# Optimization experiments

Measured on AMD Instinct MI355X. Metric: run time of the kernel, lower is better.

## Reference

```python
import jax, jax.numpy as jnp
import numpy as np

EMB_LEN = 16384
EMB_DIM = 128
BETA = 0.25
WEIGHT_DECAY = 0.01


def resize_linear(x, axis, out_size):
    # PyTorch (tri)linear interpolation, align_corners=False, separable per axis.
    in_size = x.shape[axis]
    if in_size == out_size:
        return x
    src = (jnp.arange(out_size, dtype=jnp.float32) + 0.5) * (in_size / out_size) - 0.5
    src = jnp.clip(src, 0.0, in_size - 1.0)
    i0 = jnp.floor(src).astype(jnp.int32)
    i1 = jnp.minimum(i0 + 1, in_size - 1)
    w1 = src - i0.astype(jnp.float32)
    x0 = jnp.take(x, i0, axis=axis)
    x1 = jnp.take(x, i1, axis=axis)
    bshape = [1] * x.ndim
    bshape[axis] = out_size
    w1 = w1.reshape(bshape)
    return x0 * (1.0 - w1) + x1 * w1


def setup_inputs() -> dict:
    key = jax.random.key(0)
    k1, k2 = jax.random.split(key)
    b, c, h, w = 16384, 16, 2, 4  # h*w must equal 8 (see shape analysis)
    z = jax.random.normal(k1, (b, c, h, w), dtype=jnp.float32)
    emb_weight = jax.random.uniform(
        k2, (EMB_LEN, EMB_DIM), dtype=jnp.float32,
        minval=-1.0 / EMB_LEN, maxval=1.0 / EMB_LEN)
    return {"z": z, "emb_weight": emb_weight}


def reference(z, emb_weight):
    b, c, h, w = z.shape
    # feature_unfolding: F.interpolate(x, 2, mode='trilinear') -> size=(2,2,2)
    x = z[:, :, None, :, :]                       # [b,c,1,h,w]
    x = resize_linear(x, 2, 2)                    # depth 1 -> 2 (duplicate)
    x = resize_linear(x, 3, 2)                    # h -> 2
    x = resize_linear(x, 4, 2)                    # w -> 2
    # pixelshuffle3D_downscale(scale=2) on [b,c,2,2,2] -> [b,8c,1,1,1];
    # flatten order matches contiguous reshape.
    zf = x.reshape(b, c * 8)                      # [b, emb_dim]
    # squared L2 distance via expansion
    d = (jnp.sum(zf ** 2, axis=1, keepdims=True)
         + jnp.sum(emb_weight ** 2, axis=1)
         - 2.0 * zf @ emb_weight.T)               # [b, emb_len]
    idx = jnp.argmin(d, axis=1)                   # [b]
    z_q = emb_weight[idx].reshape(b, c, h, w)
    sg = jax.lax.stop_gradient
    commit = BETA * jnp.mean((sg(z_q) - z) ** 2) + jnp.mean((z_q - sg(z)) ** 2)
    zd = sg(z)
    vx = z_q - jnp.mean(z_q)
    vy = zd - jnp.mean(zd)
    pearson = 0.5 + 0.5 * jnp.sum(vx * vy) / (
        jnp.sqrt(jnp.sum(vx ** 2)) * jnp.sqrt(jnp.sum(vy ** 2)))
    # torch.linalg.norm(W, ord=1) on 2D matrix = max column abs-sum
    reg = WEIGHT_DECAY * jnp.max(jnp.sum(jnp.abs(emb_weight), axis=0))
    loss = commit + pearson + reg
    z_q_out = z + sg(z_q - z)                     # straight-through
    # rearrange 'b h w c -> b c h w' on a [b,c,h,w] tensor == permute(0,3,1,2)
    z_q_out = jnp.transpose(z_q_out, (0, 3, 1, 2))
    return z_q_out, loss, idx
```

## Files before the change

### kernel.cpp

```cpp
#include <hip/hip_runtime.h>
#include <cstdint>
#include <cstddef>

#define B_ROWS 16384
#define EMB_LEN 16384
#define K_DIM 128
#define JSPLIT 8
#define JLEN (EMB_LEN / JSPLIT)
#define RB 32
#define JT 256
#define KC 16

typedef float v2f __attribute__((ext_vector_type(2)));

typedef const __attribute__((address_space(1))) void* gas_vp;
typedef __attribute__((address_space(3))) void* las_vp;

__device__ __forceinline__ void dma16(const float* g, float* l) {
    __builtin_amdgcn_global_load_lds((gas_vp)g, (las_vp)l, 16, 0, 0);
}

__global__ void zf_kernel(const float* __restrict__ z,
                          float* __restrict__ zf, float* __restrict__ Cb) {
    int b = blockIdx.x;
    int i = threadIdx.x;
    int c = i >> 3, h = (i >> 1) & 1, wp = i & 1;
    const float* zr = z + (size_t)b * 128 + c * 8 + h * 4 + wp * 2;
    float v = 0.5f * zr[0] + 0.5f * zr[1];
    zf[(size_t)b * 128 + i] = v;
    float s = v * v;
    for (int o = 32; o; o >>= 1) s += __shfl_down(s, o, 64);
    __shared__ float sm[2];
    if ((threadIdx.x & 63) == 0) sm[threadIdx.x >> 6] = s;
    __syncthreads();
    if (threadIdx.x == 0) Cb[b] = sm[0] + sm[1];
}

__global__ void transpose_kernel(const float* __restrict__ emb,
                                 float* __restrict__ embT) {
    __shared__ float t[128][65];
    int j0 = blockIdx.x * 64;
    int jl = threadIdx.x >> 2;
    int kq = threadIdx.x & 3;
    const float* er = emb + (size_t)(j0 + jl) * 128;
#pragma unroll
    for (int q = 0; q < 8; ++q) {
        int k4 = (kq * 8 + q) * 4;
        float4 v = *(const float4*)(er + k4);
        t[k4 + 0][jl] = v.x;
        t[k4 + 1][jl] = v.y;
        t[k4 + 2][jl] = v.z;
        t[k4 + 3][jl] = v.w;
    }
    __syncthreads();
    int kk = threadIdx.x >> 4;
    int jl4 = (threadIdx.x & 15) * 4;
#pragma unroll
    for (int q = 0; q < 8; ++q) {
        int k = kk + q * 16;
        float4 v = make_float4(t[k][jl4], t[k][jl4 + 1], t[k][jl4 + 2], t[k][jl4 + 3]);
        *(float4*)(embT + (size_t)k * EMB_LEN + j0 + jl4) = v;
    }
}

#define PK_ROW(cA, cB, av) { \
    v2f aa = {av, av}; \
    cA = __builtin_elementwise_fma(aa, b01, cA); \
    cB = __builtin_elementwise_fma(aa, b23, cB); \
}

#define UPD(rr, cA, cB) { \
    float cbr = cbs[w8 + rr]; \
    float dv0 = cbr - 2.0f * cA.x; \
    float dv1 = cbr - 2.0f * cA.y; \
    float dv2 = cbr - 2.0f * cB.x; \
    float dv3 = cbr - 2.0f * cB.y; \
    if (dv0 < bd##rr) { bd##rr = dv0; bj##rr = jb; } \
    if (dv1 < bd##rr) { bd##rr = dv1; bj##rr = jb + 1; } \
    if (dv2 < bd##rr) { bd##rr = dv2; bj##rr = jb + 2; } \
    if (dv3 < bd##rr) { bd##rr = dv3; bj##rr = jb + 3; } \
}

#define RED(rr) { \
    float bd = bd##rr; int bj = bj##rr; \
    for (int o = 32; o; o >>= 1) { \
        float d2 = __shfl_down(bd, o, 64); \
        int j2 = __shfl_down(bj, o, 64); \
        if (d2 < bd || (d2 == bd && j2 < bj)) { bd = d2; bj = j2; } \
    } \
    if (l == 0) { \
        cand_d[sp * B_ROWS + rbase + w8 + rr] = bd; \
        cand_j[sp * B_ROWS + rbase + w8 + rr] = bj; \
    } \
}

__global__ void __launch_bounds__(256)
__attribute__((amdgpu_num_vgpr(160)))
argmin_kernel(const float* __restrict__ zf,
              const float* __restrict__ Cb,
              const float* __restrict__ embT,
              float* __restrict__ cand_d,
              int* __restrict__ cand_j) {
    __shared__ float zfs[K_DIM][RB + 4];
    __shared__ float es[2][KC][JT];
    __shared__ float cbs[RB];

    int sp = blockIdx.x & 7;
    int rb = blockIdx.x >> 3;
    int rbase = rb * RB;
    int jbase = sp * JLEN;
    int tid = threadIdx.x;
    int w = tid >> 6;
    int l = tid & 63;
    int w8 = w << 3;
    int l4 = l << 2;

    {
        int r0 = tid >> 3;
        int kq0 = tid & 7;
        const float* zr = zf + (size_t)(rbase + r0) * K_DIM;
        for (int kq = kq0; kq < 32; kq += 8) {
            float4 v = *(const float4*)(zr + kq * 4);
            zfs[kq * 4 + 0][r0] = v.x;
            zfs[kq * 4 + 1][r0] = v.y;
            zfs[kq * 4 + 2][r0] = v.z;
            zfs[kq * 4 + 3][r0] = v.w;
        }
        if (tid < RB) cbs[tid] = Cb[rbase + tid];
    }

    float bd0 = 3.4e38f, bd1 = 3.4e38f, bd2 = 3.4e38f, bd3 = 3.4e38f;
    float bd4 = 3.4e38f, bd5 = 3.4e38f, bd6 = 3.4e38f, bd7 = 3.4e38f;
    int bj0 = 0, bj1 = 0, bj2 = 0, bj3 = 0, bj4 = 0, bj5 = 0, bj6 = 0, bj7 = 0;

    {
        const float* gb = embT + jbase + l4;
        float* lb = &es[0][w][0];
        dma16(gb + (size_t)(0 + w) * EMB_LEN, lb + 0 * JT);
        dma16(gb + (size_t)(4 + w) * EMB_LEN, lb + 4 * JT);
        dma16(gb + (size_t)(8 + w) * EMB_LEN, lb + 8 * JT);
        dma16(gb + (size_t)(12 + w) * EMB_LEN, lb + 12 * JT);
    }

    int buf = 0;
    for (int jt = 0; jt < JLEN; jt += JT) {
        v2f c0a = {0.f, 0.f}, c0b = {0.f, 0.f};
        v2f c1a = {0.f, 0.f}, c1b = {0.f, 0.f};
        v2f c2a = {0.f, 0.f}, c2b = {0.f, 0.f};
        v2f c3a = {0.f, 0.f}, c3b = {0.f, 0.f};
        v2f c4a = {0.f, 0.f}, c4b = {0.f, 0.f};
        v2f c5a = {0.f, 0.f}, c5b = {0.f, 0.f};
        v2f c6a = {0.f, 0.f}, c6b = {0.f, 0.f};
        v2f c7a = {0.f, 0.f}, c7b = {0.f, 0.f};

        for (int kc = 0; kc < K_DIM; kc += KC) {
            __syncthreads();

            {
                int kc2 = kc + KC, jt2 = jt;
                if (kc2 == K_DIM) { kc2 = 0; jt2 += JT; }
                if (jt2 < JLEN) {
                    const float* gb = embT + (size_t)kc2 * EMB_LEN + jbase + jt2 + l4;
                    float* lb = &es[buf ^ 1][w][0];
                    dma16(gb + (size_t)(0 + w) * EMB_LEN, lb + 0 * JT);
                    dma16(gb + (size_t)(4 + w) * EMB_LEN, lb + 4 * JT);
                    dma16(gb + (size_t)(8 + w) * EMB_LEN, lb + 8 * JT);
                    dma16(gb + (size_t)(12 + w) * EMB_LEN, lb + 12 * JT);
                }
            }

            const float (*eb)[JT] = es[buf];
#pragma unroll
            for (int k = 0; k < KC; ++k) {
                const float4 bv = *(const float4*)(&eb[k][l4]);
                const float4 a0 = *(const float4*)(&zfs[kc + k][w8]);
                const float4 a1 = *(const float4*)(&zfs[kc + k][w8 + 4]);
                v2f b01 = {bv.x, bv.y};
                v2f b23 = {bv.z, bv.w};
                PK_ROW(c0a, c0b, a0.x)
                PK_ROW(c1a, c1b, a0.y)
                PK_ROW(c2a, c2b, a0.z)
                PK_ROW(c3a, c3b, a0.w)
                PK_ROW(c4a, c4b, a1.x)
                PK_ROW(c5a, c5b, a1.y)
                PK_ROW(c6a, c6b, a1.z)
                PK_ROW(c7a, c7b, a1.w)
            }
            buf ^= 1;
        }

        int jb = jbase + jt + l4;
        UPD(0, c0a, c0b)
        UPD(1, c1a, c1b)
        UPD(2, c2a, c2b)
        UPD(3, c3a, c3b)
        UPD(4, c4a, c4b)
        UPD(5, c5a, c5b)
        UPD(6, c6a, c6b)
        UPD(7, c7a, c7b)
    }

    RED(0)
    RED(1)
    RED(2)
    RED(3)
    RED(4)
    RED(5)
    RED(6)
    RED(7)
}

__global__ void merge_kernel(const float* __restrict__ cand_d,
                             const int* __restrict__ cand_j,
                             int* __restrict__ idxw,
                             float* __restrict__ out_idx) {
    int b = blockIdx.x * 256 + threadIdx.x;
    float bd = cand_d[b];
    int bj = cand_j[b];
#pragma unroll
    for (int s = 1; s < JSPLIT; ++s) {
        float d = cand_d[s * B_ROWS + b];
        int j = cand_j[s * B_ROWS + b];
        if (d < bd) { bd = d; bj = j; }
    }
    idxw[b] = bj;
    out_idx[b] = (float)bj;
}

__global__ void output_kernel(const float* __restrict__ z,
                              const float* __restrict__ emb,
                              const int* __restrict__ idxw,
                              float* __restrict__ out,
                              double* __restrict__ accs) {
    int stride = gridDim.x * blockDim.x;
    double s[6] = {0, 0, 0, 0, 0, 0};
    for (int n = blockIdx.x * blockDim.x + threadIdx.x; n < B_ROWS * 128; n += stride) {
        int b = n >> 7, i = n & 127;
        int c = i >> 3, h = (i >> 2) & 1, w = i & 3;
        float zv = z[n];
        float qv = emb[(size_t)idxw[b] * 128 + i];
        float diff = qv - zv;
        out[(size_t)((b * 4 + w) * 16 + c) * 2 + h] = zv + diff;
        s[0] += (double)qv;
        s[1] += (double)zv;
        s[2] += (double)qv * qv;
        s[3] += (double)zv * zv;
        s[4] += (double)qv * zv;
        s[5] += (double)diff * diff;
    }
    int lane = threadIdx.x & 63, wv = threadIdx.x >> 6;
#pragma unroll
    for (int q = 0; q < 6; ++q)
        for (int o = 32; o; o >>= 1) s[q] += __shfl_down(s[q], o, 64);
    __shared__ double sm[6][4];
    if (lane == 0)
#pragma unroll
        for (int q = 0; q < 6; ++q) sm[q][wv] = s[q];
    __syncthreads();
    if (threadIdx.x == 0) {
#pragma unroll
        for (int q = 0; q < 6; ++q)
            atomicAdd(&accs[q], sm[q][0] + sm[q][1] + sm[q][2] + sm[q][3]);
    }
}

__global__ void colsum_kernel(const float* __restrict__ emb, float* __restrict__ colsum) {
    int j = blockIdx.x;
    double s = 0;
    for (int i = threadIdx.x; i < EMB_LEN; i += blockDim.x)
        s += (double)fabsf(emb[(size_t)i * 128 + j]);
    int lane = threadIdx.x & 63, wv = threadIdx.x >> 6;
    for (int o = 32; o; o >>= 1) s += __shfl_down(s, o, 64);
    __shared__ double sm[4];
    if (lane == 0) sm[wv] = s;
    __syncthreads();
    if (threadIdx.x == 0) colsum[j] = (float)(sm[0] + sm[1] + sm[2] + sm[3]);
}

__global__ void loss_kernel(const double* __restrict__ accs,
                            const float* __restrict__ colsum,
                            float* __restrict__ out_loss) {
    __shared__ float sm[128];
    int tid = threadIdx.x;
    sm[tid] = colsum[tid];
    __syncthreads();
    for (int s = 64; s; s >>= 1) {
        if (tid < s) sm[tid] = fmaxf(sm[tid], sm[tid + s]);
        __syncthreads();
    }
    if (tid == 0) {
        double n = (double)B_ROWS * 128.0;
        double m = accs[5] / n;
        double commit = 0.25 * m + m;
        double Sx = accs[0], Sy = accs[1], Sxx = accs[2], Syy = accs[3], Sxy = accs[4];
        double cov = Sxy - Sx * Sy / n;
        double vx = Sxx - Sx * Sx / n;
        double vy = Syy - Sy * Sy / n;
        double pearson = 0.5 + 0.5 * cov / (sqrt(vx) * sqrt(vy));
        double reg = 0.01 * (double)sm[0];
        out_loss[0] = (float)(commit + pearson + reg);
    }
}

extern "C" void kernel_launch(void* const* d_in, const int* in_sizes, int n_in,
                              void* d_out, int out_size, void* d_ws, size_t ws_size,
                              hipStream_t stream) {
    const float* z = (const float*)d_in[0];
    const float* emb = (const float*)d_in[1];
    float* out = (float*)d_out;

    float* zf = (float*)d_ws;
    float* embT = zf + 2097152;
    float* Cb = embT + 2097152;
    float* cand_d = Cb + 16384;
    int* cand_j = (int*)(cand_d + JSPLIT * B_ROWS);
    int* idxw = cand_j + JSPLIT * B_ROWS;
    double* accs = (double*)(idxw + 16384);
    float* colsum = (float*)(accs + 8);

    hipMemsetAsync(accs, 0, 8 * sizeof(double), stream);

    zf_kernel<<<B_ROWS, 128, 0, stream>>>(z, zf, Cb);
    transpose_kernel<<<EMB_LEN / 64, 256, 0, stream>>>(emb, embT);
    argmin_kernel<<<(B_ROWS / RB) * JSPLIT, 256, 0, stream>>>(zf, Cb, embT, cand_d, cand_j);
    merge_kernel<<<B_ROWS / 256, 256, 0, stream>>>(cand_d, cand_j, idxw, out + 2097153);
    output_kernel<<<1024, 256, 0, stream>>>(z, emb, idxw, out, accs);
    colsum_kernel<<<128, 256, 0, stream>>>(emb, colsum);
    loss_kernel<<<1, 128, 0, stream>>>(accs, colsum, out + 2097152);
}
```

Before: 1.005 ms.

## Widen per-thread tile to 8x8 columns and drop packed FMA intrinsics

Each thread now computes 8 codebook columns (two float4 groups 256 apart) for 8 rows instead of 4, doubling the JT tile to 512 while halving the K chunk to 8 so the LDS footprint stays the same. The DMA staging is remapped to fill the wider tile, and the packed v2f FMAs are replaced with scalar fmaf that the compiler may or may not pack. The aim is to raise arithmetic intensity per LDS read of the zf operand. It doubles the accumulator registers (64) under a 160-VGPR cap, which risks spills or lower occupancy, and it adds more barriers per tile because of the smaller K chunk.

```diff
diff --git a/kernel.cpp b/kernel.cpp
--- a/kernel.cpp
+++ b/kernel.cpp
@@ -8,10 +8,8 @@
 #define JSPLIT 8
 #define JLEN (EMB_LEN / JSPLIT)
 #define RB 32
-#define JT 256
-#define KC 16
-
-typedef float v2f __attribute__((ext_vector_type(2)));
+#define JT 512
+#define KC 8
 
 typedef const __attribute__((address_space(1))) void* gas_vp;
 typedef __attribute__((address_space(3))) void* las_vp;
@@ -63,22 +61,34 @@
     }
 }
 
-#define PK_ROW(cA, cB, av) { \
-    v2f aa = {av, av}; \
-    cA = __builtin_elementwise_fma(aa, b01, cA); \
-    cB = __builtin_elementwise_fma(aa, b23, cB); \
-}
+#define FMA_ROW2(cA, cB, av) \
+    cA.x = fmaf(av, bv0.x, cA.x); \
+    cA.y = fmaf(av, bv0.y, cA.y); \
+    cA.z = fmaf(av, bv0.z, cA.z); \
+    cA.w = fmaf(av, bv0.w, cA.w); \
+    cB.x = fmaf(av, bv1.x, cB.x); \
+    cB.y = fmaf(av, bv1.y, cB.y); \
+    cB.z = fmaf(av, bv1.z, cB.z); \
+    cB.w = fmaf(av, bv1.w, cB.w);
 
 #define UPD(rr, cA, cB) { \
     float cbr = cbs[w8 + rr]; \
     float dv0 = cbr - 2.0f * cA.x; \
     float dv1 = cbr - 2.0f * cA.y; \
-    float dv2 = cbr - 2.0f * cB.x; \
-    float dv3 = cbr - 2.0f * cB.y; \
+    float dv2 = cbr - 2.0f * cA.z; \
+    float dv3 = cbr - 2.0f * cA.w; \
     if (dv0 < bd##rr) { bd##rr = dv0; bj##rr = jb; } \
     if (dv1 < bd##rr) { bd##rr = dv1; bj##rr = jb + 1; } \
     if (dv2 < bd##rr) { bd##rr = dv2; bj##rr = jb + 2; } \
     if (dv3 < bd##rr) { bd##rr = dv3; bj##rr = jb + 3; } \
+    dv0 = cbr - 2.0f * cB.x; \
+    dv1 = cbr - 2.0f * cB.y; \
+    dv2 = cbr - 2.0f * cB.z; \
+    dv3 = cbr - 2.0f * cB.w; \
+    if (dv0 < bd##rr) { bd##rr = dv0; bj##rr = jb + 256; } \
+    if (dv1 < bd##rr) { bd##rr = dv1; bj##rr = jb + 257; } \
+    if (dv2 < bd##rr) { bd##rr = dv2; bj##rr = jb + 258; } \
+    if (dv3 < bd##rr) { bd##rr = dv3; bj##rr = jb + 259; } \
 }
 
 #define RED(rr) { \
@@ -135,23 +145,24 @@
 
     {
         const float* gb = embT + jbase + l4;
-        float* lb = &es[0][w][0];
-        dma16(gb + (size_t)(0 + w) * EMB_LEN, lb + 0 * JT);
-        dma16(gb + (size_t)(4 + w) * EMB_LEN, lb + 4 * JT);
-        dma16(gb + (size_t)(8 + w) * EMB_LEN, lb + 8 * JT);
-        dma16(gb + (size_t)(12 + w) * EMB_LEN, lb + 12 * JT);
+        float* lb = &es[0][0][0];
+#pragma unroll
+        for (int q = 0; q < 4; ++q) {
+            int s = q * 4 + w;
+            dma16(gb + (size_t)(s >> 1) * EMB_LEN + (s & 1) * 256, lb + s * 256);
+        }
     }
 
     int buf = 0;
     for (int jt = 0; jt < JLEN; jt += JT) {
-        v2f c0a = {0.f, 0.f}, c0b = {0.f, 0.f};
-        v2f c1a = {0.f, 0.f}, c1b = {0.f, 0.f};
-        v2f c2a = {0.f, 0.f}, c2b = {0.f, 0.f};
-        v2f c3a = {0.f, 0.f}, c3b = {0.f, 0.f};
-        v2f c4a = {0.f, 0.f}, c4b = {0.f, 0.f};
-        v2f c5a = {0.f, 0.f}, c5b = {0.f, 0.f};
-        v2f c6a = {0.f, 0.f}, c6b = {0.f, 0.f};
-        v2f c7a = {0.f, 0.f}, c7b = {0.f, 0.f};
+        float4 c0a = make_float4(0.f, 0.f, 0.f, 0.f), c0b = make_float4(0.f, 0.f, 0.f, 0.f);
+        float4 c1a = make_float4(0.f, 0.f, 0.f, 0.f), c1b = make_float4(0.f, 0.f, 0.f, 0.f);
+        float4 c2a = make_float4(0.f, 0.f, 0.f, 0.f), c2b = make_float4(0.f, 0.f, 0.f, 0.f);
+        float4 c3a = make_float4(0.f, 0.f, 0.f, 0.f), c3b = make_float4(0.f, 0.f, 0.f, 0.f);
+        float4 c4a = make_float4(0.f, 0.f, 0.f, 0.f), c4b = make_float4(0.f, 0.f, 0.f, 0.f);
+        float4 c5a = make_float4(0.f, 0.f, 0.f, 0.f), c5b = make_float4(0.f, 0.f, 0.f, 0.f);
+        float4 c6a = make_float4(0.f, 0.f, 0.f, 0.f), c6b = make_float4(0.f, 0.f, 0.f, 0.f);
+        float4 c7a = make_float4(0.f, 0.f, 0.f, 0.f), c7b = make_float4(0.f, 0.f, 0.f, 0.f);
 
         for (int kc = 0; kc < K_DIM; kc += KC) {
             __syncthreads();
@@ -161,30 +172,30 @@
                 if (kc2 == K_DIM) { kc2 = 0; jt2 += JT; }
                 if (jt2 < JLEN) {
                     const float* gb = embT + (size_t)kc2 * EMB_LEN + jbase + jt2 + l4;
-                    float* lb = &es[buf ^ 1][w][0];
-                    dma16(gb + (size_t)(0 + w) * EMB_LEN, lb + 0 * JT);
-                    dma16(gb + (size_t)(4 + w) * EMB_LEN, lb + 4 * JT);
-                    dma16(gb + (size_t)(8 + w) * EMB_LEN, lb + 8 * JT);
-                    dma16(gb + (size_t)(12 + w) * EMB_LEN, lb + 12 * JT);
+                    float* lb = &es[buf ^ 1][0][0];
+#pragma unroll
+                    for (int q = 0; q < 4; ++q) {
+                        int s = q * 4 + w;
+                        dma16(gb + (size_t)(s >> 1) * EMB_LEN + (s & 1) * 256, lb + s * 256);
+                    }
                 }
             }
 
             const float (*eb)[JT] = es[buf];
 #pragma unroll
             for (int k = 0; k < KC; ++k) {
-                const float4 bv = *(const float4*)(&eb[k][l4]);
+                const float4 bv0 = *(const float4*)(&eb[k][l4]);
+                const float4 bv1 = *(const float4*)(&eb[k][256 + l4]);
                 const float4 a0 = *(const float4*)(&zfs[kc + k][w8]);
                 const float4 a1 = *(const float4*)(&zfs[kc + k][w8 + 4]);
-                v2f b01 = {bv.x, bv.y};
-                v2f b23 = {bv.z, bv.w};
-                PK_ROW(c0a, c0b, a0.x)
-                PK_ROW(c1a, c1b, a0.y)
-                PK_ROW(c2a, c2b, a0.z)
-                PK_ROW(c3a, c3b, a0.w)
-                PK_ROW(c4a, c4b, a1.x)
-                PK_ROW(c5a, c5b, a1.y)
-                PK_ROW(c6a, c6b, a1.z)
-                PK_ROW(c7a, c7b, a1.w)
+                FMA_ROW2(c0a, c0b, a0.x)
+                FMA_ROW2(c1a, c1b, a0.y)
+                FMA_ROW2(c2a, c2b, a0.z)
+                FMA_ROW2(c3a, c3b, a0.w)
+                FMA_ROW2(c4a, c4b, a1.x)
+                FMA_ROW2(c5a, c5b, a1.y)
+                FMA_ROW2(c6a, c6b, a1.z)
+                FMA_ROW2(c7a, c7b, a1.w)
             }
             buf ^= 1;
         }
```

New measurement: 1.092 ms. 8.7% more time.
